# Kernel tuning notes

Hardware: AMD Instinct MI355X
Metric: run time of the kernel (lower is better)

## Reference

```python
import jax, jax.numpy as jnp
import numpy as np

B, N, C, H, P, L = 32, 64, 8, 64, 16, 8  # batch, nodes, commodities, hidden, max_paths, max_path_len


def setup_inputs() -> dict:
    key = jax.random.key(0)
    ks = jax.random.split(key, 8)
    edge_features = jax.random.normal(ks[0], (B, N, N, C, H), dtype=jnp.float32)
    graph_embedding = jax.random.normal(ks[1], (B, H), dtype=jnp.float32)
    selected_commodity = jax.random.randint(ks[2], (B,), 0, C, dtype=jnp.int32)
    paths = jax.random.randint(ks[3], (B, P, L), 0, N, dtype=jnp.int32)
    path_len = jnp.clip(jax.random.randint(ks[4], (B, P), 0, 9), 2, L).astype(jnp.int32)
    path_mask = jnp.ones((B, P), dtype=bool)
    W1 = jax.random.normal(ks[5], (2 * H, 128), dtype=jnp.float32) * (1.0 / np.sqrt(2 * H))
    b1 = jnp.zeros((128,), dtype=jnp.float32)
    W2 = jax.random.normal(ks[6], (128, 1), dtype=jnp.float32) * (1.0 / np.sqrt(128))
    b2 = jnp.zeros((1,), dtype=jnp.float32)
    return {"edge_features": edge_features, "graph_embedding": graph_embedding,
            "selected_commodity": selected_commodity, "paths": paths,
            "path_len": path_len, "path_mask": path_mask,
            "W1": W1, "b1": b1, "W2": W2, "b2": b2}


def reference(edge_features, graph_embedding, selected_commodity, paths, path_len,
              path_mask, W1, b1, W2, b2):
    # per-path edges (u, v): [B, P, E] with E = L - 1
    u = paths[:, :, :-1]
    v = paths[:, :, 1:]
    E = u.shape[2]
    b_idx = jnp.arange(B)[:, None, None]
    c_idx = selected_commodity[:, None, None]
    # gather edge features along each path: [B, P, E, H]
    feats = edge_features[b_idx, u, v, c_idx]
    # valid-edge mask from path lengths (paths with len<2 -> zero feature)
    emask = (jnp.arange(E)[None, None, :] < (path_len[:, :, None] - 1)).astype(feats.dtype)
    cnt = emask.sum(axis=2, keepdims=True)  # [B, P, 1]
    path_feat = (feats * emask[..., None]).sum(axis=2) / jnp.maximum(cnt, 1.0)  # [B, P, H]
    g = jnp.broadcast_to(graph_embedding[:, None, :], path_feat.shape)
    inp = jnp.concatenate([path_feat, g], axis=-1)  # [B, P, 2H]
    h = jax.nn.relu(inp @ W1 + b1)
    scores = (h @ W2 + b2)[..., 0]  # [B, P]
    neg_inf = jnp.asarray(-jnp.inf, scores.dtype)
    scores = jnp.where(path_mask, scores, neg_inf)
    action_probs = jax.nn.softmax(scores, axis=-1)
    log_probs = jax.nn.log_softmax(scores, axis=-1)
    log_probs_safe = jnp.where(path_mask, log_probs, 0.0)
    entropy = -(action_probs * log_probs_safe).sum(axis=-1)
    return (action_probs, log_probs, entropy)
```

## Files before the change

### kernel.cpp

```cpp
#include <hip/hip_runtime.h>
#include <math.h>

#define BB 32
#define NN 64
#define CC 8
#define HH 64
#define PP 16
#define LL 8

__global__ __launch_bounds__(256) void score_kernel(
    const float* __restrict__ ef,
    const float* __restrict__ ge,
    const int*   __restrict__ sc,
    const int*   __restrict__ paths,
    const int*   __restrict__ plen,
    const float* __restrict__ W1,
    const float* __restrict__ b1,
    const float* __restrict__ W2,
    const float* __restrict__ b2,
    float* __restrict__ scores)
{
    const int gw   = (blockIdx.x * blockDim.x + threadIdx.x) >> 6;
    const int lane = threadIdx.x & 63;
    const int b    = gw >> 4;
    const int p    = gw & 15;

    const int c = sc[b];

    const int* pp = paths + (b * PP + p) * LL;
    int cnt = plen[b * PP + p] - 1;
    cnt = (cnt < 1) ? 1 : (cnt > LL - 1 ? LL - 1 : cnt);
    int node[LL];
    #pragma unroll
    for (int l = 0; l < LL; ++l) node[l] = pp[l];
    float s = 0.0f;
    for (int e = 0; e < cnt; ++e) {
        int u = node[e];
        int v = node[e + 1];
        int idx = (((b * NN + u) * NN + v) * CC + c) * HH + lane;
        s += ef[idx];
    }
    const float pf = s / (float)cnt;
    const float gv = ge[b * HH + lane];

    float h1 = b1[lane];
    float h2 = b1[64 + lane];
    #pragma unroll 8
    for (int k = 0; k < 64; ++k) {
        float a = __shfl(pf, k, 64);
        h1 += a * W1[k * 128 + lane];
        h2 += a * W1[k * 128 + 64 + lane];
    }
    #pragma unroll 8
    for (int k = 0; k < 64; ++k) {
        float a = __shfl(gv, k, 64);
        h1 += a * W1[(64 + k) * 128 + lane];
        h2 += a * W1[(64 + k) * 128 + 64 + lane];
    }
    h1 = fmaxf(h1, 0.0f);
    h2 = fmaxf(h2, 0.0f);
    float cs = h1 * W2[lane] + h2 * W2[64 + lane];
    #pragma unroll
    for (int off = 32; off >= 1; off >>= 1)
        cs += __shfl_down(cs, off, 64);
    if (lane == 0) scores[b * PP + p] = cs + b2[0];
}

__global__ __launch_bounds__(64) void softmax_kernel(
    const float* __restrict__ scores,
    const int*   __restrict__ pmask,
    float* __restrict__ out)
{
    const int b    = blockIdx.x;
    const int lane = threadIdx.x & 63;
    if (lane >= PP) return;

    const bool m = pmask[b * PP + lane] != 0;
    const float s = m ? scores[b * PP + lane] : -INFINITY;

    float mx = s;
    #pragma unroll
    for (int off = 8; off >= 1; off >>= 1)
        mx = fmaxf(mx, __shfl_xor(mx, off, 64));

    const float e = m ? expf(s - mx) : 0.0f;
    float se = e;
    #pragma unroll
    for (int off = 8; off >= 1; off >>= 1)
        se += __shfl_xor(se, off, 64);

    const float prob = e / se;
    const float lse  = logf(se);
    const float lp   = (s - mx) - lse;
    const float lps  = m ? lp : 0.0f;

    float ent = -prob * lps;
    #pragma unroll
    for (int off = 8; off >= 1; off >>= 1)
        ent += __shfl_xor(ent, off, 64);

    out[b * PP + lane]           = prob;
    out[BB * PP + b * PP + lane] = lp;
    if (lane == 0) out[2 * BB * PP + b] = ent;
}

extern "C" void kernel_launch(void* const* d_in, const int* in_sizes, int n_in,
                              void* d_out, int out_size, void* d_ws, size_t ws_size,
                              hipStream_t stream) {
    const float* ef    = (const float*)d_in[0];
    const float* ge    = (const float*)d_in[1];
    const int*   sc    = (const int*)d_in[2];
    const int*   paths = (const int*)d_in[3];
    const int*   plen  = (const int*)d_in[4];
    const int*   pmask = (const int*)d_in[5];
    const float* W1    = (const float*)d_in[6];
    const float* b1    = (const float*)d_in[7];
    const float* W2    = (const float*)d_in[8];
    const float* b2    = (const float*)d_in[9];
    float*       out   = (float*)d_out;
    float*       scores = (float*)d_ws;

    score_kernel<<<(BB * PP) / 4, 256, 0, stream>>>(
        ef, ge, sc, paths, plen, W1, b1, W2, b2, scores);
    softmax_kernel<<<BB, 64, 0, stream>>>(scores, pmask, out);
}
```

Before: 315.3 us.

## Fuse path scoring and softmax into one kernel with one block per batch

Merges the score kernel and the softmax kernel into a single launch. Each 1024-thread block handles one batch row, with one wavefront per path, and passes scores through shared memory instead of a global workspace. Path nodes are now loaded as two int4 vector loads, and the edge-gather loop is fully unrolled with a predicate so the feature loads can be issued together. This removes a second kernel launch and a global round trip, but it cuts the grid to 32 large blocks, which may lower occupancy spread across CUs.

```diff
diff --git a/kernel.cpp b/kernel.cpp
--- a/kernel.cpp
+++ b/kernel.cpp
@@ -8,37 +8,43 @@
 #define PP 16
 #define LL 8
 
-__global__ __launch_bounds__(256) void score_kernel(
+__global__ __launch_bounds__(1024) void fused_kernel(
     const float* __restrict__ ef,
     const float* __restrict__ ge,
     const int*   __restrict__ sc,
     const int*   __restrict__ paths,
     const int*   __restrict__ plen,
+    const int*   __restrict__ pmask,
     const float* __restrict__ W1,
     const float* __restrict__ b1,
     const float* __restrict__ W2,
     const float* __restrict__ b2,
-    float* __restrict__ scores)
+    float* __restrict__ out)
 {
-    const int gw   = (blockIdx.x * blockDim.x + threadIdx.x) >> 6;
+    __shared__ float sl[PP];
+
+    const int b    = blockIdx.x;
+    const int wid  = threadIdx.x >> 6;
     const int lane = threadIdx.x & 63;
-    const int b    = gw >> 4;
-    const int p    = gw & 15;
 
     const int c = sc[b];
 
-    const int* pp = paths + (b * PP + p) * LL;
-    int cnt = plen[b * PP + p] - 1;
+    const int* pp = paths + (b * PP + wid) * LL;
+    int cnt = plen[b * PP + wid] - 1;
     cnt = (cnt < 1) ? 1 : (cnt > LL - 1 ? LL - 1 : cnt);
-    int node[LL];
+
+    const int4 q0 = *reinterpret_cast<const int4*>(pp);
+    const int4 q1 = *reinterpret_cast<const int4*>(pp + 4);
+    const int nd[LL] = {q0.x, q0.y, q0.z, q0.w, q1.x, q1.y, q1.z, q1.w};
+
+    float s = 0.0f;
     #pragma unroll
-    for (int l = 0; l < LL; ++l) node[l] = pp[l];
-    float s = 0.0f;
-    for (int e = 0; e < cnt; ++e) {
-        int u = node[e];
-        int v = node[e + 1];
-        int idx = (((b * NN + u) * NN + v) * CC + c) * HH + lane;
-        s += ef[idx];
+    for (int e = 0; e < LL - 1; ++e) {
+        if (e < cnt) {
+            const int u = nd[e];
+            const int v = nd[e + 1];
+            s += ef[(((b * NN + u) * NN + v) * CC + c) * HH + lane];
+        }
     }
     const float pf = s / (float)cnt;
     const float gv = ge[b * HH + lane];
@@ -47,61 +53,57 @@
     float h2 = b1[64 + lane];
     #pragma unroll 8
     for (int k = 0; k < 64; ++k) {
-        float a = __shfl(pf, k, 64);
+        const float a = __shfl(pf, k, 64);
         h1 += a * W1[k * 128 + lane];
         h2 += a * W1[k * 128 + 64 + lane];
     }
     #pragma unroll 8
     for (int k = 0; k < 64; ++k) {
-        float a = __shfl(gv, k, 64);
+        const float a = __shfl(gv, k, 64);
         h1 += a * W1[(64 + k) * 128 + lane];
         h2 += a * W1[(64 + k) * 128 + 64 + lane];
     }
     h1 = fmaxf(h1, 0.0f);
     h2 = fmaxf(h2, 0.0f);
+
     float cs = h1 * W2[lane] + h2 * W2[64 + lane];
     #pragma unroll
     for (int off = 32; off >= 1; off >>= 1)
         cs += __shfl_down(cs, off, 64);
-    if (lane == 0) scores[b * PP + p] = cs + b2[0];
-}
+    if (lane == 0) sl[wid] = cs + b2[0];
 
-__global__ __launch_bounds__(64) void softmax_kernel(
-    const float* __restrict__ scores,
-    const int*   __restrict__ pmask,
-    float* __restrict__ out)
-{
-    const int b    = blockIdx.x;
-    const int lane = threadIdx.x & 63;
-    if (lane >= PP) return;
+    __syncthreads();
 
-    const bool m = pmask[b * PP + lane] != 0;
-    const float s = m ? scores[b * PP + lane] : -INFINITY;
+    if (threadIdx.x < PP) {
+        const int p = threadIdx.x;
+        const bool m = pmask[b * PP + p] != 0;
+        const float sv = m ? sl[p] : -INFINITY;
 
-    float mx = s;
-    #pragma unroll
-    for (int off = 8; off >= 1; off >>= 1)
-        mx = fmaxf(mx, __shfl_xor(mx, off, 64));
+        float mx = sv;
+        #pragma unroll
+        for (int off = 8; off >= 1; off >>= 1)
+            mx = fmaxf(mx, __shfl_xor(mx, off, 64));
 
-    const float e = m ? expf(s - mx) : 0.0f;
-    float se = e;
-    #pragma unroll
-    for (int off = 8; off >= 1; off >>= 1)
-        se += __shfl_xor(se, off, 64);
+        const float e = m ? expf(sv - mx) : 0.0f;
+        float se = e;
+        #pragma unroll
+        for (int off = 8; off >= 1; off >>= 1)
+            se += __shfl_xor(se, off, 64);
 
-    const float prob = e / se;
-    const float lse  = logf(se);
-    const float lp   = (s - mx) - lse;
-    const float lps  = m ? lp : 0.0f;
+        const float prob = e / se;
+        const float lse  = logf(se);
+        const float lp   = (sv - mx) - lse;
+        const float lps  = m ? lp : 0.0f;
 
-    float ent = -prob * lps;
-    #pragma unroll
-    for (int off = 8; off >= 1; off >>= 1)
-        ent += __shfl_xor(ent, off, 64);
+        float ent = -prob * lps;
+        #pragma unroll
+        for (int off = 8; off >= 1; off >>= 1)
+            ent += __shfl_xor(ent, off, 64);
 
-    out[b * PP + lane]           = prob;
-    out[BB * PP + b * PP + lane] = lp;
-    if (lane == 0) out[2 * BB * PP + b] = ent;
+        out[b * PP + p]           = prob;
+        out[BB * PP + b * PP + p] = lp;
+        if (p == 0) out[2 * BB * PP + b] = ent;
+    }
 }
 
 extern "C" void kernel_launch(void* const* d_in, const int* in_sizes, int n_in,
@@ -118,9 +120,9 @@
     const float* W2    = (const float*)d_in[8];
     const float* b2    = (const float*)d_in[9];
     float*       out   = (float*)d_out;
-    float*       scores = (float*)d_ws;
 
-    score_kernel<<<(BB * PP) / 4, 256, 0, stream>>>(
-        ef, ge, sc, paths, plen, W1, b1, W2, b2, scores);
-    softmax_kernel<<<BB, 64, 0, stream>>>(scores, pmask, out);
+    (void)d_ws; (void)ws_size;
+
+    fused_kernel<<<BB, PP * 64, 0, stream>>>(
+        ef, ge, sc, paths, plen, pmask, W1, b1, W2, b2, out);
 }
```

Result: no change. 310.0 us (-1.7%).
